# Performance work log

Hardware: AMD Instinct MI355X
Metric: run time of the kernel (lower is better)

## Reference

```python
import jax, jax.numpy as jnp
import numpy as np

D_MODEL = 1024
N_HEAD = 16
D_K = D_MODEL // N_HEAD


def setup_inputs() -> dict:
    key = jax.random.key(0)
    ks = jax.random.split(key, 9)
    s = 1.0 / np.sqrt(D_MODEL)
    return {
        "x": jax.random.normal(ks[0], (2, 2048, D_MODEL), dtype=jnp.float32),
        "Wq": jax.random.uniform(ks[1], (D_MODEL, D_MODEL), jnp.float32, -s, s),
        "bq": jax.random.uniform(ks[2], (D_MODEL,), jnp.float32, -s, s),
        "Wk": jax.random.uniform(ks[3], (D_MODEL, D_MODEL), jnp.float32, -s, s),
        "bk": jax.random.uniform(ks[4], (D_MODEL,), jnp.float32, -s, s),
        "Wv": jax.random.uniform(ks[5], (D_MODEL, D_MODEL), jnp.float32, -s, s),
        "bv": jax.random.uniform(ks[6], (D_MODEL,), jnp.float32, -s, s),
        "Wo": jax.random.uniform(ks[7], (D_MODEL, D_MODEL), jnp.float32, -s, s),
        "bo": jax.random.uniform(ks[8], (D_MODEL,), jnp.float32, -s, s),
    }


def reference(x, Wq, bq, Wk, bk, Wv, bv, Wo, bo):
    B, S, D = x.shape
    # linear projections (torch Linear: x @ W.T + b)
    q = x @ Wq.T + bq
    k = x @ Wk.T + bk
    v = x @ Wv.T + bv
    # split heads: [B, H, S, d_k]
    q = q.reshape(B, S, N_HEAD, D_K).transpose(0, 2, 1, 3)
    k = k.reshape(B, S, N_HEAD, D_K).transpose(0, 2, 1, 3)
    v = v.reshape(B, S, N_HEAD, D_K).transpose(0, 2, 1, 3)
    scores = jnp.einsum("bhqd,bhkd->bhqk", q, k) / np.sqrt(D_K).astype(jnp.float32)
    attn = jax.nn.softmax(scores, axis=-1)
    out = jnp.einsum("bhqk,bhkd->bhqd", attn, v)
    out = out.transpose(0, 2, 1, 3).reshape(B, S, D)
    return out @ Wo.T + bo
```

## Files before the change

kernel.cpp:

```cpp
#include <hip/hip_runtime.h>
#include <hip/hip_bf16.h>


typedef unsigned short u16;
typedef __attribute__((ext_vector_type(4))) unsigned short u16x4;
typedef __attribute__((ext_vector_type(8))) short short8;
typedef __attribute__((ext_vector_type(4))) float f32x4;

__device__ __forceinline__ u16 f2bf(float f) {
  __bf16 b = (__bf16)f;
  return __builtin_bit_cast(unsigned short, b);
}

__device__ __forceinline__ f32x4 mfma_bf16(short8 a, short8 b, f32x4 c) {
  return __builtin_amdgcn_mfma_f32_16x16x32_bf16(a, b, c, 0, 0, 0);
}

#define GLL16(gp, lp) __builtin_amdgcn_global_load_lds( \
    (const __attribute__((address_space(1))) void*)(gp), \
    (__attribute__((address_space(3))) void*)(lp), 16, 0, 0)

#define QSCALE 0.18033688011112042f

__global__ __launch_bounds__(256) void cast_all(
    const float* __restrict__ x,
    const float* __restrict__ wq, const float* __restrict__ wk,
    const float* __restrict__ wv, const float* __restrict__ wo,
    u16* __restrict__ xb, u16* __restrict__ wqb, u16* __restrict__ wkb,
    u16* __restrict__ wvb, u16* __restrict__ wob)
{
  const int z = blockIdx.z;
  const float* s; u16* d; int n4;
  if (z == 0)      { s = x;  d = xb;  n4 = 1048576; }
  else if (z == 1) { s = wq; d = wqb; n4 = 262144; }
  else if (z == 2) { s = wk; d = wkb; n4 = 262144; }
  else if (z == 3) { s = wv; d = wvb; n4 = 262144; }
  else             { s = wo; d = wob; n4 = 262144; }
  int i = blockIdx.x * 256 + threadIdx.x;
  if (i >= n4) return;
  float4 v = ((const float4*)s)[i];
  u16x4 o; o[0] = f2bf(v.x); o[1] = f2bf(v.y); o[2] = f2bf(v.z); o[3] = f2bf(v.w);
  ((u16x4*)d)[i] = o;
}

__device__ __forceinline__ void gemm_core(const u16* __restrict__ A,
                                          const u16* __restrict__ B,
                                          int m0, int n0,
                                          u16* sA, u16* sB, f32x4 acc[4][4])
{
  const int tid = threadIdx.x;
  const int lane = tid & 63, wave = tid >> 6;
  const int wr = wave >> 1, wc = wave & 1;
  const u16* ga = A + (size_t)(m0 + (tid >> 2)) * 1024 + (tid & 3) * 8;
  const u16* gb = B + (size_t)(n0 + (tid >> 2)) * 1024 + (tid & 3) * 8;
  u16* la0 = sA + wave * 512;          u16* la1 = sA + 2048 + wave * 512;
  u16* lb0 = sB + wave * 512;          u16* lb1 = sB + 2048 + wave * 512;
  const int rl = lane & 15, kg = (lane >> 4) * 8;

  for (int k0 = 0; k0 < 1024; k0 += 32) {
    GLL16(ga + k0,             la0);
    GLL16(ga + 64 * 1024 + k0, la1);
    GLL16(gb + k0,             lb0);
    GLL16(gb + 64 * 1024 + k0, lb1);
    __syncthreads();
    short8 af[4], bf_[4];
#pragma unroll
    for (int m = 0; m < 4; ++m) af[m]  = *(const short8*)&sA[(wr * 64 + m * 16 + rl) * 32 + kg];
#pragma unroll
    for (int n = 0; n < 4; ++n) bf_[n] = *(const short8*)&sB[(wc * 64 + n * 16 + rl) * 32 + kg];
#pragma unroll
    for (int m = 0; m < 4; ++m)
#pragma unroll
      for (int n = 0; n < 4; ++n)
        acc[m][n] = mfma_bf16(af[m], bf_[n], acc[m][n]);
    __syncthreads();
  }
}

__global__ __launch_bounds__(256) void gemm_qkv(
    const u16* __restrict__ X, const u16* __restrict__ Wqkv,
    const float* __restrict__ bq, const float* __restrict__ bk, const float* __restrict__ bv,
    u16* __restrict__ Qo, u16* __restrict__ Ko, u16* __restrict__ Vt)
{
  __shared__ u16 sA[4096], sB[4096];
  const int bflat = blockIdx.x;
  const int xcd = bflat & 7, idx = bflat >> 3;
  const int m0 = (xcd * 4 + (idx & 3)) * 128;
  const int nt = idx >> 2;
  const int z = nt >> 3;
  const int n0 = (nt & 7) * 128;
  const float* bias = (z == 0) ? bq : (z == 1) ? bk : bv;

  f32x4 acc[4][4];
#pragma unroll
  for (int m = 0; m < 4; ++m)
#pragma unroll
    for (int n = 0; n < 4; ++n) acc[m][n] = (f32x4){0.f, 0.f, 0.f, 0.f};

  gemm_core(X, Wqkv, m0, nt * 128, sA, sB, acc);

  const int lane = threadIdx.x & 63, wave = threadIdx.x >> 6;
  const int wr = wave >> 1, wc = wave & 1;
  const int rl = lane & 15, rg = (lane >> 4) * 4;

  if (z < 2) {
    u16* dst = (z == 0) ? Qo : Ko;
    const float cs = (z == 0) ? QSCALE : 1.0f;
#pragma unroll
    for (int n = 0; n < 4; ++n) {
      int col = n0 + wc * 64 + n * 16 + rl;
      float bb = bias[col];
#pragma unroll
      for (int m = 0; m < 4; ++m) {
        int row0 = m0 + wr * 64 + m * 16 + rg;
#pragma unroll
        for (int r = 0; r < 4; ++r)
          dst[(size_t)(row0 + r) * 1024 + col] = f2bf((acc[m][n][r] + bb) * cs);
      }
    }
  } else {
#pragma unroll
    for (int n = 0; n < 4; ++n) {
      int col = n0 + wc * 64 + n * 16 + rl;
      float bb = bias[col];
#pragma unroll
      for (int m = 0; m < 4; ++m) {
        int row0 = m0 + wr * 64 + m * 16 + rg;
        int bidx = row0 >> 11, sl = row0 & 2047;
        u16x4 pk;
#pragma unroll
        for (int r = 0; r < 4; ++r) pk[r] = f2bf(acc[m][n][r] + bb);
        *(u16x4*)&Vt[((size_t)(bidx * 1024 + col)) * 2048 + sl] = pk;
      }
    }
  }
}

__global__ __launch_bounds__(256) void gemm_out(
    const u16* __restrict__ Ob, const u16* __restrict__ Wob,
    const float* __restrict__ bo, float* __restrict__ Out)
{
  __shared__ u16 sA[2048], sB[4096];
  const int bflat = blockIdx.x;
  const int xcd = bflat & 7, idx = bflat >> 3;
  const int m0 = (xcd * 8 + (idx & 7)) * 64;
  const int n0 = (idx >> 3) * 128;

  const int tid = threadIdx.x, lane = tid & 63, wave = tid >> 6;
  const int wr = wave >> 1, wc = wave & 1;
  const u16* ga = Ob  + (size_t)(m0 + (tid >> 2)) * 1024 + (tid & 3) * 8;
  const u16* gb = Wob + (size_t)(n0 + (tid >> 2)) * 1024 + (tid & 3) * 8;
  u16* la0 = sA + wave * 512;
  u16* lb0 = sB + wave * 512;          u16* lb1 = sB + 2048 + wave * 512;
  const int rl = lane & 15, kg = (lane >> 4) * 8, rg = (lane >> 4) * 4;

  f32x4 acc[2][4];
#pragma unroll
  for (int m = 0; m < 2; ++m)
#pragma unroll
    for (int n = 0; n < 4; ++n) acc[m][n] = (f32x4){0.f, 0.f, 0.f, 0.f};

  for (int k0 = 0; k0 < 1024; k0 += 32) {
    GLL16(ga + k0,             la0);
    GLL16(gb + k0,             lb0);
    GLL16(gb + 64 * 1024 + k0, lb1);
    __syncthreads();
    short8 af[2], bf_[4];
#pragma unroll
    for (int m = 0; m < 2; ++m) af[m]  = *(const short8*)&sA[(wr * 32 + m * 16 + rl) * 32 + kg];
#pragma unroll
    for (int n = 0; n < 4; ++n) bf_[n] = *(const short8*)&sB[(wc * 64 + n * 16 + rl) * 32 + kg];
#pragma unroll
    for (int m = 0; m < 2; ++m)
#pragma unroll
      for (int n = 0; n < 4; ++n)
        acc[m][n] = mfma_bf16(af[m], bf_[n], acc[m][n]);
    __syncthreads();
  }

#pragma unroll
  for (int n = 0; n < 4; ++n) {
    int col = n0 + wc * 64 + n * 16 + rl;
    float bb = bo[col];
#pragma unroll
    for (int m = 0; m < 2; ++m) {
      int row0 = m0 + wr * 32 + m * 16 + rg;
#pragma unroll
      for (int r = 0; r < 4; ++r)
        Out[(size_t)(row0 + r) * 1024 + col] = acc[m][n][r] + bb;
    }
  }
}

__global__ __launch_bounds__(512) void attn_fwd(
    const u16* __restrict__ Q, const u16* __restrict__ K,
    const u16* __restrict__ Vt, u16* __restrict__ O)
{
  __shared__ u16 sK[2][64][64];
  __shared__ u16 sV[2][64][64];

  const int tid = threadIdx.x, lane = tid & 63, wave = tid >> 6;
  const int rl = lane & 15, g = lane >> 4;

  const int bflat = blockIdx.x;
  const int xcd = bflat & 7, j = bflat >> 3;
  const int bh = xcd * 4 + (j >> 4);
  const int qchunk = j & 15;
  const int b = bh >> 4, h = bh & 15;
  const int qbase = qchunk * 128 + wave * 16;

  const u16* Qp = Q + (size_t)(b * 2048 + qbase) * 1024 + h * 64;
  const u16* Kp = K + (size_t)(b * 2048) * 1024 + h * 64;
  const u16* Vp = Vt + (size_t)(bh * 64) * 2048;

  short8 qf[2];
#pragma unroll
  for (int hf = 0; hf < 2; ++hf)
    qf[hf] = *(const short8*)&Qp[(size_t)rl * 1024 + hf * 32 + g * 8];

  const int keyperm = 8 * (rl >> 2) + (rl & 3);
  const int swzK8 = (((rl & 3) | (((rl >> 2) & 1) << 2))) * 8;
  const int swzV8 = (rl & 7) * 8;

  const int srow = lane >> 3;
  const int feK = (((lane & 7) ^ (srow & 3)) * 8) ^ ((wave & 1) * 32);
  const int feV = (((lane & 7) ^ srow) * 8);

  f32x4 oacc[4];
  f32x4 lacc = (f32x4){0.f, 0.f, 0.f, 0.f};
#pragma unroll
  for (int dg = 0; dg < 4; ++dg) oacc[dg] = (f32x4){0.f, 0.f, 0.f, 0.f};
  float mrun = -INFINITY;

  const short8 ONES = {0x3F80, 0x3F80, 0x3F80, 0x3F80,
                       0x3F80, 0x3F80, 0x3F80, 0x3F80};

  auto stage = [&](int nb, int kt) {
    const int grow = wave * 8 + srow;
    GLL16(Kp + (size_t)(kt + grow) * 1024 + feK, &sK[nb][wave * 8][0]);
    GLL16(Vp + (size_t)grow * 2048 + kt + feV,   &sV[nb][wave * 8][0]);
  };

  auto proc_sub = [&](int nb, int sub) {
    short8 kf[2][2];
#pragma unroll
    for (int t = 0; t < 2; ++t) {
      const int r = sub * 32 + keyperm + 4 * t;
#pragma unroll
      for (int hf = 0; hf < 2; ++hf)
        kf[t][hf] = *(const short8*)&sK[nb][r][(hf * 32 + g * 8) ^ swzK8];
    }
    short8 vf[4];
#pragma unroll
    for (int dg = 0; dg < 4; ++dg)
      vf[dg] = *(const short8*)&sV[nb][dg * 16 + rl][(sub * 32 + g * 8) ^ swzV8];

    f32x4 sc[2];
    __builtin_amdgcn_s_setprio(1);
#pragma unroll
    for (int t = 0; t < 2; ++t) {
      f32x4 a = (f32x4){0.f, 0.f, 0.f, 0.f};
      a = mfma_bf16(kf[t][0], qf[0], a);
      a = mfma_bf16(kf[t][1], qf[1], a);
      sc[t] = a;
    }
    __builtin_amdgcn_s_setprio(0);

    float p2[8];
#pragma unroll
    for (int t = 0; t < 2; ++t)
#pragma unroll
      for (int r = 0; r < 4; ++r) p2[t * 4 + r] = sc[t][r];
    float a0 = fmaxf(fmaxf(p2[0], p2[1]), p2[2]);
    float a1 = fmaxf(fmaxf(p2[3], p2[4]), p2[5]);
    float a2 = fmaxf(p2[6], p2[7]);
    float tm = fmaxf(fmaxf(a0, a1), a2);
    if (!__all(tm <= mrun + 8.0f)) {
      tm = fmaxf(tm, __shfl_xor(tm, 16));
      tm = fmaxf(tm, __shfl_xor(tm, 32));
      float mnew = fmaxf(mrun, tm);
      float sfac = __builtin_amdgcn_exp2f(mrun - mnew);
      mrun = mnew;
#pragma unroll
      for (int dg = 0; dg < 4; ++dg)
#pragma unroll
        for (int r = 0; r < 4; ++r) oacc[dg][r] *= sfac;
      lacc[0] *= sfac;
    }
    short8 pb;
#pragma unroll
    for (int j2 = 0; j2 < 8; ++j2)
      pb[j2] = (short)f2bf(__builtin_amdgcn_exp2f(p2[j2] - mrun));

    __builtin_amdgcn_s_setprio(1);
    lacc = mfma_bf16(ONES, pb, lacc);
#pragma unroll
    for (int dg = 0; dg < 4; ++dg)
      oacc[dg] = mfma_bf16(vf[dg], pb, oacc[dg]);
    __builtin_amdgcn_s_setprio(0);
  };

  stage(0, 0);
  __syncthreads();
  for (int kt = 0; kt < 2048; kt += 128) {
    stage(1, kt + 64);
    proc_sub(0, 0);
    proc_sub(0, 1);
    __syncthreads();
    if (kt + 128 < 2048) stage(0, kt + 128);
    proc_sub(1, 0);
    proc_sub(1, 1);
    __syncthreads();
  }

  float inv = 1.0f / lacc[0];
  int qrow = qbase + rl;
  u16* op = O + (size_t)(b * 2048 + qrow) * 1024 + h * 64;
#pragma unroll
  for (int dg = 0; dg < 4; ++dg) {
    u16x4 pk;
#pragma unroll
    for (int r = 0; r < 4; ++r) pk[r] = f2bf(oacc[dg][r] * inv);
    *(u16x4*)&op[dg * 16 + g * 4] = pk;
  }
}

extern "C" void kernel_launch(void* const* d_in, const int* in_sizes, int n_in,
                              void* d_out, int out_size, void* d_ws, size_t ws_size,
                              hipStream_t stream) {
  const float* x  = (const float*)d_in[0];
  const float* Wq = (const float*)d_in[1];
  const float* bq = (const float*)d_in[2];
  const float* Wk = (const float*)d_in[3];
  const float* bk = (const float*)d_in[4];
  const float* Wv = (const float*)d_in[5];
  const float* bv = (const float*)d_in[6];
  const float* Wo = (const float*)d_in[7];
  const float* bo = (const float*)d_in[8];

  char* ws = (char*)d_ws;
  const size_t MB = 1024 * 1024;
  u16* Xb  = (u16*)(ws + 0 * MB);
  u16* Wqb = (u16*)(ws + 8 * MB);
  u16* Wkb = (u16*)(ws + 10 * MB);
  u16* Wvb = (u16*)(ws + 12 * MB);
  u16* Wob = (u16*)(ws + 14 * MB);
  u16* Qb  = (u16*)(ws + 16 * MB);
  u16* Kb  = (u16*)(ws + 24 * MB);
  u16* Vtb = (u16*)(ws + 32 * MB);
  u16* Ob  = (u16*)(ws + 40 * MB);

  cast_all<<<dim3(4096, 1, 5), 256, 0, stream>>>(x, Wq, Wk, Wv, Wo,
                                                 Xb, Wqb, Wkb, Wvb, Wob);
  gemm_qkv<<<dim3(768), 256, 0, stream>>>(Xb, Wqb, bq, bk, bv, Qb, Kb, Vtb);
  attn_fwd<<<dim3(512), 512, 0, stream>>>(Qb, Kb, Vtb, Ob);
  gemm_out<<<dim3(512), 256, 0, stream>>>(Ob, Wob, bo, (float*)d_out);
}
```

Baseline: 121.6 us.

## Double-buffer LDS tiles in projection GEMMs to overlap loads with MFMA

Both the QKV projection GEMM and the output projection GEMM now use two LDS buffers. The next K-slice is issued via global_load_lds before the MFMAs on the current slice run, so global-to-LDS latency can be hidden behind compute. Each step now has one explicit vmcnt wait and one barrier instead of two __syncthreads. LDS usage per block doubles, which may lower occupancy. The attention kernel is unchanged.

```diff
diff --git a/kernel.cpp b/kernel.cpp
--- a/kernel.cpp
+++ b/kernel.cpp
@@ -19,6 +19,9 @@
 #define GLL16(gp, lp) __builtin_amdgcn_global_load_lds( \
     (const __attribute__((address_space(1))) void*)(gp), \
     (__attribute__((address_space(3))) void*)(lp), 16, 0, 0)
+
+#define WAITV0 asm volatile("s_waitcnt vmcnt(0)" ::: "memory")
+#define BAR __builtin_amdgcn_s_barrier()
 
 #define QSCALE 0.18033688011112042f
 
@@ -53,27 +56,41 @@
   const int wr = wave >> 1, wc = wave & 1;
   const u16* ga = A + (size_t)(m0 + (tid >> 2)) * 1024 + (tid & 3) * 8;
   const u16* gb = B + (size_t)(n0 + (tid >> 2)) * 1024 + (tid & 3) * 8;
-  u16* la0 = sA + wave * 512;          u16* la1 = sA + 2048 + wave * 512;
-  u16* lb0 = sB + wave * 512;          u16* lb1 = sB + 2048 + wave * 512;
+  const int lofs = wave * 512;
   const int rl = lane & 15, kg = (lane >> 4) * 8;
 
-  for (int k0 = 0; k0 < 1024; k0 += 32) {
-    GLL16(ga + k0,             la0);
-    GLL16(ga + 64 * 1024 + k0, la1);
-    GLL16(gb + k0,             lb0);
-    GLL16(gb + 64 * 1024 + k0, lb1);
-    __syncthreads();
+  auto stageb = [&](int nb, int k0) {
+    u16* a = sA + nb * 4096 + lofs;
+    u16* b = sB + nb * 4096 + lofs;
+    GLL16(ga + k0,             a);
+    GLL16(ga + 64 * 1024 + k0, a + 2048);
+    GLL16(gb + k0,             b);
+    GLL16(gb + 64 * 1024 + k0, b + 2048);
+  };
+  auto compute = [&](int nb) {
+    const u16* bA = sA + nb * 4096;
+    const u16* bB = sB + nb * 4096;
     short8 af[4], bf_[4];
 #pragma unroll
-    for (int m = 0; m < 4; ++m) af[m]  = *(const short8*)&sA[(wr * 64 + m * 16 + rl) * 32 + kg];
-#pragma unroll
-    for (int n = 0; n < 4; ++n) bf_[n] = *(const short8*)&sB[(wc * 64 + n * 16 + rl) * 32 + kg];
+    for (int m = 0; m < 4; ++m) af[m]  = *(const short8*)&bA[(wr * 64 + m * 16 + rl) * 32 + kg];
+#pragma unroll
+    for (int n = 0; n < 4; ++n) bf_[n] = *(const short8*)&bB[(wc * 64 + n * 16 + rl) * 32 + kg];
 #pragma unroll
     for (int m = 0; m < 4; ++m)
 #pragma unroll
       for (int n = 0; n < 4; ++n)
         acc[m][n] = mfma_bf16(af[m], bf_[n], acc[m][n]);
-    __syncthreads();
+  };
+
+  stageb(0, 0);
+  WAITV0; BAR;
+  for (int t = 0; t < 32; t += 2) {
+    stageb(1, (t + 1) * 32);
+    compute(0);
+    WAITV0; BAR;
+    if (t + 2 < 32) stageb(0, (t + 2) * 32);
+    compute(1);
+    WAITV0; BAR;
   }
 }
 
@@ -82,7 +99,7 @@
     const float* __restrict__ bq, const float* __restrict__ bk, const float* __restrict__ bv,
     u16* __restrict__ Qo, u16* __restrict__ Ko, u16* __restrict__ Vt)
 {
-  __shared__ u16 sA[4096], sB[4096];
+  __shared__ u16 sA[8192], sB[8192];
   const int bflat = blockIdx.x;
   const int xcd = bflat & 7, idx = bflat >> 3;
   const int m0 = (xcd * 4 + (idx & 3)) * 128;
@@ -140,7 +157,7 @@
     const u16* __restrict__ Ob, const u16* __restrict__ Wob,
     const float* __restrict__ bo, float* __restrict__ Out)
 {
-  __shared__ u16 sA[2048], sB[4096];
+  __shared__ u16 sA[4096], sB[8192];
   const int bflat = blockIdx.x;
   const int xcd = bflat & 7, idx = bflat >> 3;
   const int m0 = (xcd * 8 + (idx & 7)) * 64;
@@ -150,8 +167,7 @@
   const int wr = wave >> 1, wc = wave & 1;
   const u16* ga = Ob  + (size_t)(m0 + (tid >> 2)) * 1024 + (tid & 3) * 8;
   const u16* gb = Wob + (size_t)(n0 + (tid >> 2)) * 1024 + (tid & 3) * 8;
-  u16* la0 = sA + wave * 512;
-  u16* lb0 = sB + wave * 512;          u16* lb1 = sB + 2048 + wave * 512;
+  const int lofs = wave * 512;
   const int rl = lane & 15, kg = (lane >> 4) * 8, rg = (lane >> 4) * 4;
 
   f32x4 acc[2][4];
@@ -160,22 +176,35 @@
 #pragma unroll
     for (int n = 0; n < 4; ++n) acc[m][n] = (f32x4){0.f, 0.f, 0.f, 0.f};
 
-  for (int k0 = 0; k0 < 1024; k0 += 32) {
-    GLL16(ga + k0,             la0);
-    GLL16(gb + k0,             lb0);
-    GLL16(gb + 64 * 1024 + k0, lb1);
-    __syncthreads();
+  auto stageb = [&](int nb, int k0) {
+    GLL16(ga + k0,             sA + nb * 2048 + lofs);
+    GLL16(gb + k0,             sB + nb * 4096 + lofs);
+    GLL16(gb + 64 * 1024 + k0, sB + nb * 4096 + 2048 + lofs);
+  };
+  auto compute = [&](int nb) {
+    const u16* bA = sA + nb * 2048;
+    const u16* bB = sB + nb * 4096;
     short8 af[2], bf_[4];
 #pragma unroll
-    for (int m = 0; m < 2; ++m) af[m]  = *(const short8*)&sA[(wr * 32 + m * 16 + rl) * 32 + kg];
-#pragma unroll
-    for (int n = 0; n < 4; ++n) bf_[n] = *(const short8*)&sB[(wc * 64 + n * 16 + rl) * 32 + kg];
+    for (int m = 0; m < 2; ++m) af[m]  = *(const short8*)&bA[(wr * 32 + m * 16 + rl) * 32 + kg];
+#pragma unroll
+    for (int n = 0; n < 4; ++n) bf_[n] = *(const short8*)&bB[(wc * 64 + n * 16 + rl) * 32 + kg];
 #pragma unroll
     for (int m = 0; m < 2; ++m)
 #pragma unroll
       for (int n = 0; n < 4; ++n)
         acc[m][n] = mfma_bf16(af[m], bf_[n], acc[m][n]);
-    __syncthreads();
+  };
+
+  stageb(0, 0);
+  WAITV0; BAR;
+  for (int t = 0; t < 32; t += 2) {
+    stageb(1, (t + 1) * 32);
+    compute(0);
+    WAITV0; BAR;
+    if (t + 2 < 32) stageb(0, (t + 2) * 32);
+    compute(1);
+    WAITV0; BAR;
   }
 
 #pragma unroll
```

New measurement: 127.0 us. +4.5%, slower.

## Rewrite QKV GEMM with 256x256 tiles, double-buffered swizzled LDS, 8 waves

Applied to the files above, without the earlier changes.

Replaces the single-buffered 128x128 QKV projection GEMM with a 256x256 tile kernel using 512 threads, a 64-wide K step, and double-buffered LDS. Global-to-LDS loads for the next tile are interleaved with MFMA work on the current one. An XOR swizzle is applied to the LDS layout to avoid bank conflicts, and s_setprio raises priority around MFMA bursts. This aims to hide memory latency and raise data reuse, at the cost of 128KB of LDS per block, fewer blocks (192 on a device with more CUs), and heavy register pressure.

```diff
diff --git a/kernel.cpp b/kernel.cpp
--- a/kernel.cpp
+++ b/kernel.cpp
@@ -43,93 +43,151 @@
   ((u16x4*)d)[i] = o;
 }
 
-__device__ __forceinline__ void gemm_core(const u16* __restrict__ A,
-                                          const u16* __restrict__ B,
-                                          int m0, int n0,
-                                          u16* sA, u16* sB, f32x4 acc[4][4])
-{
-  const int tid = threadIdx.x;
-  const int lane = tid & 63, wave = tid >> 6;
-  const int wr = wave >> 1, wc = wave & 1;
-  const u16* ga = A + (size_t)(m0 + (tid >> 2)) * 1024 + (tid & 3) * 8;
-  const u16* gb = B + (size_t)(n0 + (tid >> 2)) * 1024 + (tid & 3) * 8;
-  u16* la0 = sA + wave * 512;          u16* la1 = sA + 2048 + wave * 512;
-  u16* lb0 = sB + wave * 512;          u16* lb1 = sB + 2048 + wave * 512;
-  const int rl = lane & 15, kg = (lane >> 4) * 8;
-
-  for (int k0 = 0; k0 < 1024; k0 += 32) {
-    GLL16(ga + k0,             la0);
-    GLL16(ga + 64 * 1024 + k0, la1);
-    GLL16(gb + k0,             lb0);
-    GLL16(gb + 64 * 1024 + k0, lb1);
-    __syncthreads();
-    short8 af[4], bf_[4];
-#pragma unroll
-    for (int m = 0; m < 4; ++m) af[m]  = *(const short8*)&sA[(wr * 64 + m * 16 + rl) * 32 + kg];
-#pragma unroll
-    for (int n = 0; n < 4; ++n) bf_[n] = *(const short8*)&sB[(wc * 64 + n * 16 + rl) * 32 + kg];
-#pragma unroll
-    for (int m = 0; m < 4; ++m)
-#pragma unroll
-      for (int n = 0; n < 4; ++n)
-        acc[m][n] = mfma_bf16(af[m], bf_[n], acc[m][n]);
-    __syncthreads();
-  }
-}
-
-__global__ __launch_bounds__(256) void gemm_qkv(
+__global__ __launch_bounds__(512, 2) void gemm_qkv(
     const u16* __restrict__ X, const u16* __restrict__ Wqkv,
     const float* __restrict__ bq, const float* __restrict__ bk, const float* __restrict__ bv,
     u16* __restrict__ Qo, u16* __restrict__ Ko, u16* __restrict__ Vt)
 {
-  __shared__ u16 sA[4096], sB[4096];
+  __shared__ u16 smem[65536];
+  u16* const sA0 = smem;
+  u16* const sA1 = smem + 16384;
+  u16* const sB0 = smem + 32768;
+  u16* const sB1 = smem + 49152;
+
+  const int tid = threadIdx.x, lane = tid & 63, w = tid >> 6;
+  const int wr = w >> 2, wcn = w & 3;
+  const int rl = lane & 15, g = lane >> 4, rsw = rl & 7;
+
   const int bflat = blockIdx.x;
   const int xcd = bflat & 7, idx = bflat >> 3;
-  const int m0 = (xcd * 4 + (idx & 3)) * 128;
-  const int nt = idx >> 2;
-  const int z = nt >> 3;
-  const int n0 = (nt & 7) * 128;
-  const float* bias = (z == 0) ? bq : (z == 1) ? bk : bv;
-
-  f32x4 acc[4][4];
-#pragma unroll
-  for (int m = 0; m < 4; ++m)
-#pragma unroll
-    for (int n = 0; n < 4; ++n) acc[m][n] = (f32x4){0.f, 0.f, 0.f, 0.f};
-
-  gemm_core(X, Wqkv, m0, nt * 128, sA, sB, acc);
-
-  const int lane = threadIdx.x & 63, wave = threadIdx.x >> 6;
-  const int wr = wave >> 1, wc = wave & 1;
-  const int rl = lane & 15, rg = (lane >> 4) * 4;
-
+  const int mt = xcd * 2 + (idx & 1);
+  const int nt = idx >> 1;
+  const int m0 = mt * 256;
+  const int z = nt >> 2;
+  const int colbase = (nt & 3) * 256;
+
+  const int lr = lane >> 3, lc = lane & 7;
+  const size_t srcoff = (size_t)(w * 8 + lr) * 1024 + ((lc ^ lr) * 8);
+  const u16* gaS = X    + (size_t)m0 * 1024 + srcoff;
+  const u16* gbS = Wqkv + (size_t)(nt * 256) * 1024 + srcoff;
+
+  f32x4 acc[8][4];
+#pragma unroll
+  for (int mf = 0; mf < 8; ++mf)
+#pragma unroll
+    for (int nf = 0; nf < 4; ++nf) acc[mf][nf] = (f32x4){0.f, 0.f, 0.f, 0.f};
+
+  auto loadA = [&](const u16* buf, int mf, int kh) -> short8 {
+    return *(const short8*)&buf[(wr * 128 + mf * 16 + rl) * 64 +
+                                (((kh * 4 + g) ^ rsw) * 8)];
+  };
+  auto loadB = [&](const u16* buf, int nf, int kh) -> short8 {
+    return *(const short8*)&buf[(wcn * 64 + nf * 16 + rl) * 64 +
+                                (((kh * 4 + g) ^ rsw) * 8)];
+  };
+
+  auto proc_tile = [&](const u16* bufA, const u16* bufB,
+                       u16* stA, u16* stB, int ts, bool doSt) {
+    short8 af[4], bf[4];
+    if (doSt) {
+#pragma unroll
+      for (int i = 0; i < 4; ++i)
+        GLL16(gaS + (size_t)(i * 64) * 1024 + ts * 64, stA + (i * 64 + w * 8) * 64);
+    }
+#pragma unroll
+    for (int nf = 0; nf < 4; ++nf) bf[nf] = loadB(bufB, nf, 0);
+#pragma unroll
+    for (int i = 0; i < 4; ++i) af[i] = loadA(bufA, i, 0);
+    __builtin_amdgcn_s_setprio(1);
+#pragma unroll
+    for (int i = 0; i < 4; ++i)
+#pragma unroll
+      for (int nf = 0; nf < 4; ++nf)
+        acc[i][nf] = mfma_bf16(af[i], bf[nf], acc[i][nf]);
+    __builtin_amdgcn_s_setprio(0);
+    __builtin_amdgcn_s_barrier();
+    if (doSt) {
+#pragma unroll
+      for (int i = 0; i < 4; ++i)
+        GLL16(gbS + (size_t)(i * 64) * 1024 + ts * 64, stB + (i * 64 + w * 8) * 64);
+    }
+#pragma unroll
+    for (int i = 0; i < 4; ++i) af[i] = loadA(bufA, 4 + i, 0);
+    __builtin_amdgcn_s_setprio(1);
+#pragma unroll
+    for (int i = 0; i < 4; ++i)
+#pragma unroll
+      for (int nf = 0; nf < 4; ++nf)
+        acc[4 + i][nf] = mfma_bf16(af[i], bf[nf], acc[4 + i][nf]);
+    __builtin_amdgcn_s_setprio(0);
+    __builtin_amdgcn_s_barrier();
+#pragma unroll
+    for (int nf = 0; nf < 4; ++nf) bf[nf] = loadB(bufB, nf, 1);
+#pragma unroll
+    for (int i = 0; i < 4; ++i) af[i] = loadA(bufA, i, 1);
+    __builtin_amdgcn_s_setprio(1);
+#pragma unroll
+    for (int i = 0; i < 4; ++i)
+#pragma unroll
+      for (int nf = 0; nf < 4; ++nf)
+        acc[i][nf] = mfma_bf16(af[i], bf[nf], acc[i][nf]);
+    __builtin_amdgcn_s_setprio(0);
+    __builtin_amdgcn_s_barrier();
+#pragma unroll
+    for (int i = 0; i < 4; ++i) af[i] = loadA(bufA, 4 + i, 1);
+    __builtin_amdgcn_s_setprio(1);
+#pragma unroll
+    for (int i = 0; i < 4; ++i)
+#pragma unroll
+      for (int nf = 0; nf < 4; ++nf)
+        acc[4 + i][nf] = mfma_bf16(af[i], bf[nf], acc[4 + i][nf]);
+    __builtin_amdgcn_s_setprio(0);
+  };
+
+#pragma unroll
+  for (int i = 0; i < 4; ++i) {
+    GLL16(gaS + (size_t)(i * 64) * 1024, sA0 + (i * 64 + w * 8) * 64);
+    GLL16(gbS + (size_t)(i * 64) * 1024, sB0 + (i * 64 + w * 8) * 64);
+  }
+  __syncthreads();
+
+#pragma unroll 1
+  for (int tt = 0; tt < 8; ++tt) {
+    proc_tile(sA0, sB0, sA1, sB1, 2 * tt + 1, true);
+    __syncthreads();
+    proc_tile(sA1, sB1, sA0, sB0, 2 * tt + 2, tt < 7);
+    __syncthreads();
+  }
+
+  const int rg = g * 4;
   if (z < 2) {
     u16* dst = (z == 0) ? Qo : Ko;
     const float cs = (z == 0) ? QSCALE : 1.0f;
-#pragma unroll
-    for (int n = 0; n < 4; ++n) {
-      int col = n0 + wc * 64 + n * 16 + rl;
+    const float* bias = (z == 0) ? bq : bk;
+#pragma unroll
+    for (int nf = 0; nf < 4; ++nf) {
+      int col = colbase + wcn * 64 + nf * 16 + rl;
       float bb = bias[col];
 #pragma unroll
-      for (int m = 0; m < 4; ++m) {
-        int row0 = m0 + wr * 64 + m * 16 + rg;
+      for (int mf = 0; mf < 8; ++mf) {
+        int row0 = m0 + wr * 128 + mf * 16 + rg;
 #pragma unroll
         for (int r = 0; r < 4; ++r)
-          dst[(size_t)(row0 + r) * 1024 + col] = f2bf((acc[m][n][r] + bb) * cs);
+          dst[(size_t)(row0 + r) * 1024 + col] = f2bf((acc[mf][nf][r] + bb) * cs);
       }
     }
   } else {
 #pragma unroll
-    for (int n = 0; n < 4; ++n) {
-      int col = n0 + wc * 64 + n * 16 + rl;
-      float bb = bias[col];
-#pragma unroll
-      for (int m = 0; m < 4; ++m) {
-        int row0 = m0 + wr * 64 + m * 16 + rg;
+    for (int nf = 0; nf < 4; ++nf) {
+      int col = colbase + wcn * 64 + nf * 16 + rl;
+      float bb = bv[col];
+#pragma unroll
+      for (int mf = 0; mf < 8; ++mf) {
+        int row0 = m0 + wr * 128 + mf * 16 + rg;
         int bidx = row0 >> 11, sl = row0 & 2047;
         u16x4 pk;
 #pragma unroll
-        for (int r = 0; r < 4; ++r) pk[r] = f2bf(acc[m][n][r] + bb);
+        for (int r = 0; r < 4; ++r) pk[r] = f2bf(acc[mf][nf][r] + bb);
         *(u16x4*)&Vt[((size_t)(bidx * 1024 + col)) * 2048 + sl] = pk;
       }
     }
@@ -352,7 +410,7 @@
 
   cast_all<<<dim3(4096, 1, 5), 256, 0, stream>>>(x, Wq, Wk, Wv, Wo,
                                                  Xb, Wqb, Wkb, Wvb, Wob);
-  gemm_qkv<<<dim3(768), 256, 0, stream>>>(Xb, Wqb, bq, bk, bv, Qb, Kb, Vtb);
+  gemm_qkv<<<dim3(192), 512, 0, stream>>>(Xb, Wqb, bq, bk, bv, Qb, Kb, Vtb);
   attn_fwd<<<dim3(512), 512, 0, stream>>>(Qb, Kb, Vtb, Ob);
   gemm_out<<<dim3(512), 256, 0, stream>>>(Ob, Wob, bo, (float*)d_out);
 }
```

After: 110.5 us. 1.1x faster.
